# Performance work log

Hardware: AMD Instinct MI355X
Metric: run time of the kernel (lower is better)

The kernel has to match this reference:

```python
import jax, jax.numpy as jnp
import numpy as np

B, SEQ, DIM = 2, 2048, 1024
HEADS, DIM_HEAD = 16, 64
INNER = HEADS * DIM_HEAD
SCALE = DIM_HEAD ** -0.5


def rotate_half(x):
    # pair consecutive dims (d r) with r=2: (x1, x2) -> (-x2, x1)
    xp = x.reshape(*x.shape[:-1], -1, 2)
    x1, x2 = xp[..., 0], xp[..., 1]
    return jnp.stack((-x2, x1), axis=-1).reshape(x.shape)


def apply_rotary_emb(freqs, t):
    # freqs: [n, rot_dim] angles; t: [b, h, n, d]
    rot_dim = freqs.shape[-1]
    t_rot, t_pass = t[..., :rot_dim], t[..., rot_dim:]
    t_rot = t_rot * jnp.cos(freqs) + rotate_half(t_rot) * jnp.sin(freqs)
    return jnp.concatenate([t_rot, t_pass], axis=-1)


def setup_inputs() -> dict:
    key = jax.random.key(0)
    ks = jax.random.split(key, 4)
    x = jax.random.normal(ks[0], (B, SEQ, DIM), dtype=jnp.float32)
    mask = jnp.ones((B, SEQ), dtype=bool)
    rotary_pos_emb = jax.random.uniform(ks[1], (SEQ, DIM_HEAD), dtype=jnp.float32)
    Wqkv = jax.random.normal(ks[2], (DIM, 3 * INNER), dtype=jnp.float32) * 0.02
    Wout = jax.random.normal(ks[3], (INNER, DIM), dtype=jnp.float32) * 0.02
    bout = jnp.zeros((DIM,), dtype=jnp.float32)
    return {"x": x, "mask": mask, "rotary_pos_emb": rotary_pos_emb,
            "Wqkv": Wqkv, "Wout": Wout, "bout": bout}


def reference(x, mask, rotary_pos_emb, Wqkv, Wout, bout):
    b, n, _ = x.shape
    qkv = x @ Wqkv                                   # [b, n, 3*inner]
    q, k, v = jnp.split(qkv, 3, axis=-1)

    def to_heads(t):
        return t.reshape(b, n, HEADS, DIM_HEAD).transpose(0, 2, 1, 3)  # [b,h,n,d]

    q, k, v = to_heads(q), to_heads(k), to_heads(v)
    freqs = rotary_pos_emb[:n, :]
    # NB: original applies rotary to q, k AND v
    q = apply_rotary_emb(freqs, q)
    k = apply_rotary_emb(freqs, k)
    v = apply_rotary_emb(freqs, v)
    q = q * SCALE

    dots = jnp.einsum('bhid,bhjd->bhij', q, k)       # [b,h,n,n]
    mask_value = -jnp.finfo(dots.dtype).max
    pad = mask[:, None, None, :]                     # [b,1,1,n] keep where True
    dots = jnp.where(pad, dots, mask_value)
    idx = jnp.arange(n)
    causal = idx[None, :] > idx[:, None]             # j >= i + (j-i+1) with i==j==n
    dots = jnp.where(causal[None, None], mask_value, dots)

    attn = jax.nn.softmax(dots, axis=-1)
    out = jnp.einsum('bhij,bhjd->bhid', attn, v)     # [b,h,n,d]
    out = out.transpose(0, 2, 1, 3).reshape(b, n, INNER)
    return out @ Wout + bout
```

## Files before the change

### kernel.cpp

```cpp
#include <hip/hip_runtime.h>
#include <hip/hip_bf16.h>
#include <stdint.h>

#define DEVI __device__ __forceinline__

typedef __bf16 bf16x8 __attribute__((ext_vector_type(8)));
typedef float f32x4 __attribute__((ext_vector_type(4)));
typedef float f32x16 __attribute__((ext_vector_type(16)));

static constexpr int SEQ = 2048;
static constexpr int DIM = 1024;
static constexpr int HEADS = 16;
static constexpr int NQKV = 3072;
static constexpr int MROWS = 4096;
static constexpr float QSCALE = 0.125f;
static constexpr float LOG2E = 1.4426950408889634f;

DEVI unsigned short f2bf(float f) {
  unsigned int u = __builtin_bit_cast(unsigned int, f);
  u += 0x7FFFu + ((u >> 16) & 1u);
  return (unsigned short)(u >> 16);
}

DEVI bf16x8 ld8(const unsigned short* p) {
  return __builtin_bit_cast(bf16x8, *(const uint4*)p);
}

DEVI f32x4 mfma16(bf16x8 a, bf16x8 b, f32x4 c) {
  return __builtin_amdgcn_mfma_f32_16x16x32_bf16(a, b, c, 0, 0, 0);
}

DEVI f32x16 mfma32(bf16x8 a, bf16x8 b, f32x16 c) {
  return __builtin_amdgcn_mfma_f32_32x32x16_bf16(a, b, c, 0, 0, 0);
}

DEVI void load_lds16(const void* g, void* l) {
  __builtin_amdgcn_global_load_lds((const __attribute__((address_space(1))) void*)g,
                                   (__attribute__((address_space(3))) void*)l,
                                   16, 0, 0);
}

DEVI int swz(int row, int kelem) {
  return row * 64 + (kelem ^ ((row & 7) << 3));
}

DEVI unsigned cvtpk(float lo, float hi) {
  unsigned r;
  asm("v_cvt_pk_bf16_f32 %0, %1, %2" : "=v"(r) : "v"(lo), "v"(hi));
  return r;
}

DEVI void pl32swap(unsigned& a, unsigned& b) {
  asm volatile("v_permlane32_swap_b32 %0, %1" : "+v"(a), "+v"(b));
}
DEVI float xhalf_max(float v) { return fmaxf(v, __shfl_xor(v, 32)); }
DEVI float xhalf_sum(float v) { return v + __shfl_xor(v, 32); }

DEVI void transpose_tile(const float* __restrict__ in, unsigned short* __restrict__ out,
                         int Kd, int Nd, int bx, int by, int tid,
                         unsigned short (*T)[68]) {
  const int n0 = bx * 64, k0 = by * 64;
  const int rr = tid >> 4, cc = (tid & 15) * 4;
#pragma unroll
  for (int p = 0; p < 4; ++p) {
    const int r = p * 16 + rr;
    float4 f = *(const float4*)(in + (size_t)(k0 + r) * Nd + n0 + cc);
    T[r][cc + 0] = f2bf(f.x);
    T[r][cc + 1] = f2bf(f.y);
    T[r][cc + 2] = f2bf(f.z);
    T[r][cc + 3] = f2bf(f.w);
  }
  __syncthreads();
#pragma unroll
  for (int p = 0; p < 4; ++p) {
    const int rn = p * 16 + rr;
    ushort4 v;
    v.x = T[cc + 0][rn];
    v.y = T[cc + 1][rn];
    v.z = T[cc + 2][rn];
    v.w = T[cc + 3][rn];
    *(ushort4*)(out + (size_t)(n0 + rn) * Kd + k0 + cc) = v;
  }
}

__global__ __launch_bounds__(256) void k_prep(
    const float* __restrict__ x, unsigned short* __restrict__ xb,
    const float* __restrict__ rope, float* __restrict__ cosb, float* __restrict__ sinb,
    const float* __restrict__ Wqkv, unsigned short* __restrict__ wqkvt,
    const float* __restrict__ Wout, unsigned short* __restrict__ woutt) {
  __shared__ unsigned short T[64][68];
  const int bid = blockIdx.x, tid = threadIdx.x;
  if (bid < 4096) {
    const int i = bid * 256 + tid;
    float4 f = *(const float4*)(x + (size_t)i * 4);
    ushort4 v;
    v.x = f2bf(f.x); v.y = f2bf(f.y); v.z = f2bf(f.z); v.w = f2bf(f.w);
    *(ushort4*)(xb + (size_t)i * 4) = v;
  } else if (bid < 4608) {
    const int i = (bid - 4096) * 256 + tid;
    float f = rope[i];
    cosb[i] = cosf(f);
    sinb[i] = sinf(f);
  } else if (bid < 5376) {
    const int idx = bid - 4608;
    transpose_tile(Wqkv, wqkvt, DIM, NQKV, idx % 48, idx / 48, tid, T);
  } else {
    const int idx = bid - 5376;
    transpose_tile(Wout, woutt, DIM, DIM, idx % 16, idx / 16, tid, T);
  }
}

DEVI void gemm_mainloop64(const unsigned short* __restrict__ A,
                          const unsigned short* __restrict__ B, int K,
                          int m0, int n0,
                          unsigned short* As, unsigned short* Bs,
                          f32x4 (&acc)[4][4]) {
  const int lane = threadIdx.x & 63;
  const int wid = threadIdx.x >> 6;
  const int wm = wid >> 1, wn = wid & 1;
  const int rsub = lane >> 3;
  const int ksw = ((lane & 7) ^ rsub) * 8;
  for (int kt = 0; kt < K; kt += 64) {
    __syncthreads();
#pragma unroll
    for (int i = 0; i < 4; ++i) {
      const int chunk = wid * 4 + i;
      const int row = chunk * 8 + rsub;
      load_lds16(A + (size_t)(m0 + row) * K + kt + ksw, As + chunk * 512);
      load_lds16(B + (size_t)(n0 + row) * K + kt + ksw, Bs + chunk * 512);
    }
    __syncthreads();
#pragma unroll
    for (int kk = 0; kk < 2; ++kk) {
      bf16x8 af[4], bfv[4];
#pragma unroll
      for (int mi = 0; mi < 4; ++mi)
        af[mi] = ld8(&As[swz(wm * 64 + mi * 16 + (lane & 15),
                             kk * 32 + 8 * (lane >> 4))]);
#pragma unroll
      for (int ni = 0; ni < 4; ++ni)
        bfv[ni] = ld8(&Bs[swz(wn * 64 + ni * 16 + (lane & 15),
                              kk * 32 + 8 * (lane >> 4))]);
#pragma unroll
      for (int mi = 0; mi < 4; ++mi)
#pragma unroll
        for (int ni = 0; ni < 4; ++ni)
          acc[mi][ni] = mfma16(af[mi], bfv[ni], acc[mi][ni]);
    }
  }
}

__global__ __launch_bounds__(512, 1) void k_gemm_qkv(
    const unsigned short* __restrict__ xb, const unsigned short* __restrict__ wt,
    const float* __restrict__ cosb, const float* __restrict__ sinb,
    unsigned short* __restrict__ qb, unsigned short* __restrict__ kb,
    unsigned short* __restrict__ vb) {
  __shared__ __align__(16) unsigned short Ab[2][2][8192];
  __shared__ __align__(16) unsigned short Bb[2][12288];
  const int tid = threadIdx.x, lane = tid & 63, wid = tid >> 6;
  const int wm = wid >> 2, wn = wid & 3;
  const int m0 = blockIdx.x * 256, n0 = blockIdx.y * 192;
  const int la15 = lane & 15, l16 = lane >> 4;
  const int pS0 = tid, pS1 = tid + 512;
  const int sr0 = pS0 >> 3, sr1 = pS1 >> 3;
  const int sc0 = ((pS0 & 7) ^ (sr0 & 7)) * 8, sc1 = ((pS1 & 7) ^ (sr1 & 7)) * 8;
  const int bsr = tid >> 3;
  const int bsc = ((tid & 7) ^ (bsr & 7)) * 8;

  auto stageA = [&](int h, int s) {
    const unsigned short* src = xb + (size_t)(m0 + h * 128) * DIM + s * 64;
    unsigned short* dst = &Ab[s & 1][h][0];
    load_lds16(src + (size_t)sr0 * DIM + sc0, dst + pS0 * 8);
    load_lds16(src + (size_t)sr1 * DIM + sc1, dst + pS1 * 8);
  };
  auto stageB3 = [&](int t, int s) {
    const unsigned short* src = wt + (size_t)(n0 + t * 64 + bsr) * DIM + s * 64;
    load_lds16(src + bsc, &Bb[s & 1][t * 4096] + tid * 8);
  };

  f32x4 acc[8][3] = {};
  stageA(0, 0); stageA(1, 0); stageB3(0, 0); stageB3(1, 0); stageB3(2, 0);
  stageA(0, 1); stageA(1, 1); stageB3(0, 1); stageB3(1, 1); stageB3(2, 1);

#pragma unroll 1
  for (int s = 0; s < 16; ++s) {
    const unsigned short* Ah = &Ab[s & 1][wm][0];
    const unsigned short* Bh = &Bb[s & 1][0];
    const int rb = wn * 48;
    bf16x8 bfr[3][2];
#pragma unroll
    for (int q = 0; q < 4; ++q) {
      if (q == 0) {
        if (s == 0)       asm volatile("s_waitcnt vmcnt(7)" ::: "memory");
        else if (s == 15) asm volatile("s_waitcnt vmcnt(0)" ::: "memory");
        else              asm volatile("s_waitcnt vmcnt(3)" ::: "memory");
        __syncthreads();
      }
      if (q == 2) __syncthreads();
      bf16x8 afr[2][2];
      if (q == 0) {
#pragma unroll
        for (int ni = 0; ni < 3; ++ni)
#pragma unroll
          for (int kk = 0; kk < 2; ++kk)
            bfr[ni][kk] = ld8(&Bh[swz(rb + ni * 16 + la15, kk * 32 + 8 * l16)]);
      }
#pragma unroll
      for (int mi = 0; mi < 2; ++mi)
#pragma unroll
        for (int kk = 0; kk < 2; ++kk)
          afr[mi][kk] = ld8(&Ah[swz(q * 32 + mi * 16 + la15, kk * 32 + 8 * l16)]);
      if (q == 0)      { if (s >= 1 && s + 1 < 16) stageA(0, s + 1); }
      else if (q == 1) { if (s >= 1 && s + 1 < 16) stageA(1, s + 1); }
      else if (q == 2) { if (s + 2 < 16) stageB3(0, s + 2); }
      else             { if (s + 2 < 16) { stageB3(1, s + 2); stageB3(2, s + 2); } }
      asm volatile("s_waitcnt lgkmcnt(0)" ::: "memory");
      __builtin_amdgcn_sched_barrier(0);
      __builtin_amdgcn_s_setprio(1);
#pragma unroll
      for (int kk = 0; kk < 2; ++kk)
#pragma unroll
        for (int mi = 0; mi < 2; ++mi)
#pragma unroll
          for (int ni = 0; ni < 3; ++ni)
            acc[2 * q + mi][ni] = mfma16(afr[mi][kk], bfr[ni][kk], acc[2 * q + mi][ni]);
      __builtin_amdgcn_s_setprio(0);
    }
  }

#pragma unroll
  for (int mq = 0; mq < 8; ++mq) {
#pragma unroll
    for (int ni = 0; ni < 3; ++ni) {
      const int ng = n0 + wn * 48 + ni * 16 + la15;
      const int d = ng & 63;
      const int part = ng >> 10;
      const int h = (ng & 1023) >> 6;
      const int mg0 = m0 + wm * 128 + mq * 16 + 4 * l16;
      const int s0 = mg0 & (SEQ - 1), b = mg0 >> 11;
      const size_t bh = (size_t)(b * HEADS + h);
      if (part == 2) {
        ushort4 vv;
#pragma unroll
        for (int r = 0; r < 4; ++r) {
          const int s = s0 + r;
          float v = acc[mq][ni][r];
          float p = __shfl_xor(v, 1);
          float cv = cosb[(s << 6) + d], sv = sinb[(s << 6) + d];
          float rot = v * cv + ((d & 1) ? p : -p) * sv;
          ((unsigned short*)&vv)[r] = f2bf(rot);
        }
        *(ushort4*)(vb + (bh * 64 + d) * SEQ + s0) = vv;
      } else {
#pragma unroll
        for (int r = 0; r < 4; ++r) {
          const int s = s0 + r;
          float v = acc[mq][ni][r];
          float p = __shfl_xor(v, 1);
          float cv = cosb[(s << 6) + d], sv = sinb[(s << 6) + d];
          float rot = v * cv + ((d & 1) ? p : -p) * sv;
          if (part == 0) {
            qb[(bh * SEQ + s) * 64 + d] = f2bf(rot * (QSCALE * LOG2E));
          } else {
            kb[(bh * SEQ + s) * 64 + d] = f2bf(rot);
          }
        }
      }
    }
  }
}

__global__ __launch_bounds__(256) void k_flash(
    const unsigned short* __restrict__ qb, const unsigned short* __restrict__ kb,
    const unsigned short* __restrict__ vtb, unsigned short* __restrict__ ao) {
  __shared__ __align__(16) unsigned short Ks[2][2][4096];
  __shared__ __align__(16) unsigned short Vt[2][4096];
  const int bh = blockIdx.x;
  const int qt = 31 - blockIdx.y;
  const int tid = threadIdx.x, lane = tid & 63, wid = tid >> 6;
  const int wq = wid >> 1, wk = wid & 1;
  const int la31 = lane & 31, h = lane >> 5;
  const unsigned short* kbh = kb + (size_t)bh * SEQ * 64;
  const unsigned short* vbh = vtb + (size_t)bh * 64 * SEQ;
  const int b = bh >> 4, hh = bh & 15;
  const int sslot = ((lane & 7) ^ (lane >> 3)) * 8;
  float* mrg = (float*)&Ks[0][0][0];
  const int mbase = wq * 2176;

  auto stageK = [&](int buf, int t) {
    const int kv0 = t * 64;
#pragma unroll
    for (int i = 0; i < 4; ++i) {
      const int chunk = wq * 4 + i;
      const int row = chunk * 8 + (lane >> 3);
      load_lds16(kbh + ((size_t)(kv0 + row) << 6) + sslot, &Ks[buf][wk][chunk * 512]);
    }
  };
  auto stageV = [&](int t) {
    const int kv0 = t * 64;
#pragma unroll
    for (int i = 0; i < 4; ++i) {
      const int chunk = wq * 4 + i;
      const int row = chunk * 8 + (lane >> 3);
      load_lds16(vbh + (size_t)row * SEQ + kv0 + sslot, &Vt[wk][chunk * 512]);
    }
  };

  const int q0 = qt * 64 + wq * 32;
  const int qr = q0 + la31;
  const unsigned short* qp = qb + ((size_t)bh * SEQ + qr) * 64;
  bf16x8 qf0 = ld8(qp + 0 + 8 * h);
  bf16x8 qf1 = ld8(qp + 16 + 8 * h);
  bf16x8 qf2 = ld8(qp + 32 + 8 * h);
  bf16x8 qf3 = ld8(qp + 48 + 8 * h);

  f32x16 o0 = {}, o1 = {};
  float m = -1e30f, l = 0.f;
  const int nkv = qt + 1;
  const int nst = (nkv + 1) >> 1;

  if (wk < nkv) stageK(0, wk);
#pragma unroll 1
  for (int st = 0; st < nst; ++st) {
    const int cur = st & 1;
    const int t = 2 * st + wk;
    const bool live = (t < nkv);
    __syncthreads();
    if (live) stageV(t);
    { const int tn = 2 * (st + 1) + wk; if (tn < nkv) stageK(cur ^ 1, tn); }

    f32x16 st0 = {}, st1 = {};
    bf16x8 pa0, pa1, pa2, pa3;
    if (live) {
      const int kv0 = t * 64;
      const unsigned short* Kc = &Ks[cur][wk][0];
      __builtin_amdgcn_s_setprio(1);
#pragma unroll
      for (int ks = 0; ks < 4; ++ks) {
        bf16x8 qk = (ks == 0) ? qf0 : (ks == 1) ? qf1 : (ks == 2) ? qf2 : qf3;
        st0 = mfma32(ld8(&Kc[swz(la31, 16 * ks + 8 * h)]), qk, st0);
        st1 = mfma32(ld8(&Kc[swz(32 + la31, 16 * ks + 8 * h)]), qk, st1);
      }
      __builtin_amdgcn_s_setprio(0);
      if (kv0 + 63 > q0) {
#pragma unroll
        for (int r = 0; r < 16; ++r) {
          const int kvo = (r & 3) + 8 * (r >> 2) + 4 * h;
          st0[r] = (kv0 + kvo > qr) ? -1e30f : st0[r];
          st1[r] = (kv0 + 32 + kvo > qr) ? -1e30f : st1[r];
        }
      }
      float a8[8];
#pragma unroll
      for (int i = 0; i < 8; ++i)
        a8[i] = fmaxf(fmaxf(st0[i], st0[i + 8]), fmaxf(st1[i], st1[i + 8]));
      float a4_0 = fmaxf(a8[0], a8[4]), a4_1 = fmaxf(a8[1], a8[5]);
      float a4_2 = fmaxf(a8[2], a8[6]), a4_3 = fmaxf(a8[3], a8[7]);
      float pmax = fmaxf(fmaxf(a4_0, a4_1), fmaxf(a4_2, a4_3));
      const bool nor = __all(pmax <= m + 8.f);
      float scl = 1.f;
      if (!nor) {
        const float rowmax = xhalf_max(pmax);
        const float mnew = fmaxf(m, rowmax);
        scl = exp2f(m - mnew);
        m = mnew;
      }
#pragma unroll
      for (int r = 0; r < 16; ++r) {
        st0[r] = exp2f(st0[r] - m);
        st1[r] = exp2f(st1[r] - m);
      }
      float s8[8];
#pragma unroll
      for (int i = 0; i < 8; ++i)
        s8[i] = (st0[i] + st0[i + 8]) + (st1[i] + st1[i + 8]);
      float s4_0 = s8[0] + s8[4], s4_1 = s8[1] + s8[5];
      float s4_2 = s8[2] + s8[6], s4_3 = s8[3] + s8[7];
      float psum = (s4_0 + s4_1) + (s4_2 + s4_3);
      const float rowsum = xhalf_sum(psum);
      if (nor) {
        l += rowsum;
      } else {
        l = l * scl + rowsum;
#pragma unroll
        for (int r = 0; r < 16; ++r) { o0[r] *= scl; o1[r] *= scl; }
      }
      unsigned w0 = cvtpk(st0[0], st0[1]),   w1 = cvtpk(st0[2], st0[3]);
      unsigned w2 = cvtpk(st0[4], st0[5]),   w3 = cvtpk(st0[6], st0[7]);
      unsigned w4 = cvtpk(st0[8], st0[9]),   w5 = cvtpk(st0[10], st0[11]);
      unsigned w6 = cvtpk(st0[12], st0[13]), w7 = cvtpk(st0[14], st0[15]);
      pl32swap(w0, w2); pl32swap(w1, w3); pl32swap(w4, w6); pl32swap(w5, w7);
      pa0 = __builtin_bit_cast(bf16x8, (uint4){w0, w1, w2, w3});
      pa1 = __builtin_bit_cast(bf16x8, (uint4){w4, w5, w6, w7});
      unsigned x0 = cvtpk(st1[0], st1[1]),   x1 = cvtpk(st1[2], st1[3]);
      unsigned x2 = cvtpk(st1[4], st1[5]),   x3 = cvtpk(st1[6], st1[7]);
      unsigned x4 = cvtpk(st1[8], st1[9]),   x5 = cvtpk(st1[10], st1[11]);
      unsigned x6 = cvtpk(st1[12], st1[13]), x7 = cvtpk(st1[14], st1[15]);
      pl32swap(x0, x2); pl32swap(x1, x3); pl32swap(x4, x6); pl32swap(x5, x7);
      pa2 = __builtin_bit_cast(bf16x8, (uint4){x0, x1, x2, x3});
      pa3 = __builtin_bit_cast(bf16x8, (uint4){x4, x5, x6, x7});
    }
    __syncthreads();
    if (live) {
      const unsigned short* Vc = &Vt[wk][0];
      __builtin_amdgcn_s_setprio(1);
      o0 = mfma32(ld8(&Vc[swz(la31, 0 + 8 * h)]), pa0, o0);
      o0 = mfma32(ld8(&Vc[swz(la31, 16 + 8 * h)]), pa1, o0);
      o0 = mfma32(ld8(&Vc[swz(la31, 32 + 8 * h)]), pa2, o0);
      o0 = mfma32(ld8(&Vc[swz(la31, 48 + 8 * h)]), pa3, o0);
      o1 = mfma32(ld8(&Vc[swz(32 + la31, 0 + 8 * h)]), pa0, o1);
      o1 = mfma32(ld8(&Vc[swz(32 + la31, 16 + 8 * h)]), pa1, o1);
      o1 = mfma32(ld8(&Vc[swz(32 + la31, 32 + 8 * h)]), pa2, o1);
      o1 = mfma32(ld8(&Vc[swz(32 + la31, 48 + 8 * h)]), pa3, o1);
      __builtin_amdgcn_s_setprio(0);
    }
  }

  __syncthreads();
  if (wk == 1) {
#pragma unroll
    for (int s = 0; s < 8; ++s) {
      f32x4 c;
      if (s < 4) { c[0]=o0[4*s]; c[1]=o0[4*s+1]; c[2]=o0[4*s+2]; c[3]=o0[4*s+3]; }
      else       { c[0]=o1[4*(s-4)]; c[1]=o1[4*(s-4)+1]; c[2]=o1[4*(s-4)+2]; c[3]=o1[4*(s-4)+3]; }
      *(f32x4*)&mrg[mbase + lane * 32 + 4 * (s ^ (lane & 7))] = c;
    }
    mrg[mbase + 2048 + lane] = m;
    mrg[mbase + 2112 + lane] = l;
  }
  __syncthreads();
  if (wk == 0) {
    const float m1 = mrg[mbase + 2048 + lane];
    const float l1 = mrg[mbase + 2112 + lane];
    const float mM = fmaxf(m, m1);
    const float sc0 = exp2f(m - mM), sc1 = exp2f(m1 - mM);
    const float lt = l * sc0 + l1 * sc1;
    const float rl = __builtin_amdgcn_rcpf(lt);
    unsigned short* aor = ao + ((size_t)(b * SEQ + qr)) * 1024 + hh * 64;
#pragma unroll
    for (int s = 0; s < 8; ++s) {
      f32x4 c = *(const f32x4*)&mrg[mbase + lane * 32 + 4 * (s ^ (lane & 7))];
      float v0, v1, v2, v3;
      if (s < 4) {
        v0 = (o0[4*s]   * sc0 + c[0] * sc1) * rl;
        v1 = (o0[4*s+1] * sc0 + c[1] * sc1) * rl;
        v2 = (o0[4*s+2] * sc0 + c[2] * sc1) * rl;
        v3 = (o0[4*s+3] * sc0 + c[3] * sc1) * rl;
      } else {
        v0 = (o1[4*(s-4)]   * sc0 + c[0] * sc1) * rl;
        v1 = (o1[4*(s-4)+1] * sc0 + c[1] * sc1) * rl;
        v2 = (o1[4*(s-4)+2] * sc0 + c[2] * sc1) * rl;
        v3 = (o1[4*(s-4)+3] * sc0 + c[3] * sc1) * rl;
      }
      uint2 uv;
      uv.x = cvtpk(v0, v1);
      uv.y = cvtpk(v2, v3);
      *(uint2*)(aor + (s < 4 ? 8 * s : 32 + 8 * (s - 4)) + 4 * h) = uv;
    }
  }
}

__global__ __launch_bounds__(256) void k_gemm_out(
    const unsigned short* __restrict__ ao, const unsigned short* __restrict__ wt,
    const float* __restrict__ bout, float* __restrict__ out) {
  __shared__ __align__(16) unsigned short As[128 * 64];
  __shared__ __align__(16) unsigned short Bs[128 * 64];
  const int m0 = blockIdx.x * 128, n0 = blockIdx.y * 128;
  f32x4 acc[4][4] = {};
  gemm_mainloop64(ao, wt, DIM, m0, n0, As, Bs, acc);
  const int lane = threadIdx.x & 63, wid = threadIdx.x >> 6;
  const int wm = wid >> 1, wn = wid & 1;
#pragma unroll
  for (int mi = 0; mi < 4; ++mi) {
#pragma unroll
    for (int ni = 0; ni < 4; ++ni) {
      const int ng = n0 + wn * 64 + ni * 16 + (lane & 15);
      const float bn = bout[ng];
#pragma unroll
      for (int r = 0; r < 4; ++r) {
        const int mg = m0 + wm * 64 + mi * 16 + 4 * (lane >> 4) + r;
        out[(size_t)mg * DIM + ng] = acc[mi][ni][r] + bn;
      }
    }
  }
}

extern "C" void kernel_launch(void* const* d_in, const int* in_sizes, int n_in,
                              void* d_out, int out_size, void* d_ws, size_t ws_size,
                              hipStream_t stream) {
  const float* x    = (const float*)d_in[0];
  const float* rope = (const float*)d_in[2];
  const float* Wqkv = (const float*)d_in[3];
  const float* Wout = (const float*)d_in[4];
  const float* bout = (const float*)d_in[5];
  float* out = (float*)d_out;

  char* ws = (char*)d_ws;
  unsigned short* xb    = (unsigned short*)(ws + 0);
  unsigned short* wqkvt = (unsigned short*)(ws + 8388608);
  unsigned short* woutt = (unsigned short*)(ws + 14680064);
  float*          cosb  = (float*)(ws + 16777216);
  float*          sinb  = (float*)(ws + 17301504);
  unsigned short* qbuf  = (unsigned short*)(ws + 17825792);
  unsigned short* kbuf  = (unsigned short*)(ws + 26214400);
  unsigned short* vbuf  = (unsigned short*)(ws + 34603008);
  unsigned short* aob   = (unsigned short*)(ws + 42991616);

  k_prep<<<5632, 256, 0, stream>>>(x, xb, rope, cosb, sinb, Wqkv, wqkvt, Wout, woutt);
  k_gemm_qkv<<<dim3(16, 16), 512, 0, stream>>>(xb, wqkvt, cosb, sinb,
                                               qbuf, kbuf, vbuf);
  k_flash<<<dim3(32, 32), 256, 0, stream>>>(qbuf, kbuf, vbuf, aob);
  k_gemm_out<<<dim3(MROWS / 128, DIM / 128), 256, 0, stream>>>(aob, woutt, bout, out);
}
```

Measured before the change: 120.9 us.

## Split long causal flash tiles across two blocks and merge partials in a new kernel

The upper 16 query tiles (which have the most KV tiles under the causal mask) are now each split into two blocks that process halves of the KV range. Each half writes a bf16 partial output plus row max and sum into reused workspace buffers. A new merge kernel combines the two partials into the attention output. The goal is to balance work across blocks and cut the long-tail critical path. The cost is an extra launch, extra global traffic, and bf16 rounding of the unnormalized partials.

```diff
diff --git a/kernel.cpp b/kernel.cpp
--- a/kernel.cpp
+++ b/kernel.cpp
@@ -272,11 +272,20 @@
 
 __global__ __launch_bounds__(256) void k_flash(
     const unsigned short* __restrict__ qb, const unsigned short* __restrict__ kb,
-    const unsigned short* __restrict__ vtb, unsigned short* __restrict__ ao) {
+    const unsigned short* __restrict__ vtb, unsigned short* __restrict__ ao,
+    unsigned short* __restrict__ pO, float* __restrict__ pM,
+    float* __restrict__ pL) {
   __shared__ __align__(16) unsigned short Ks[2][2][4096];
   __shared__ __align__(16) unsigned short Vt[2][4096];
   const int bh = blockIdx.x;
-  const int qt = 31 - blockIdx.y;
+  const int y = blockIdx.y;
+  const bool split = (y < 32);
+  const int qt = split ? (31 - (y >> 1)) : (47 - y);
+  const int half = y & 1;
+  const int nkv = qt + 1;
+  const int nlo = (nkv + 1) >> 1;
+  const int t0 = (split && half) ? nlo : 0;
+  const int nkvl = split ? (half ? nkv - nlo : nlo) : nkv;
   const int tid = threadIdx.x, lane = tid & 63, wid = tid >> 6;
   const int wq = wid >> 1, wk = wid & 1;
   const int la31 = lane & 31, h = lane >> 5;
@@ -316,24 +325,24 @@
 
   f32x16 o0 = {}, o1 = {};
   float m = -1e30f, l = 0.f;
-  const int nkv = qt + 1;
-  const int nst = (nkv + 1) >> 1;
-
-  if (wk < nkv) stageK(0, wk);
+  const int nstl = (nkvl + 1) >> 1;
+
+  if (wk < nkvl) stageK(0, t0 + wk);
 #pragma unroll 1
-  for (int st = 0; st < nst; ++st) {
-    const int cur = st & 1;
-    const int t = 2 * st + wk;
-    const bool live = (t < nkv);
+  for (int stp = 0; stp < nstl; ++stp) {
+    const int cur = stp & 1;
+    const int tl = 2 * stp + wk;
+    const bool live = (tl < nkvl);
+    const int tg = t0 + tl;
     __syncthreads();
-    if (live) stageV(t);
-    { const int tn = 2 * (st + 1) + wk; if (tn < nkv) stageK(cur ^ 1, tn); }
-
-    f32x16 st0 = {}, st1 = {};
+    if (live) stageV(tg);
+    { const int tn = 2 * (stp + 1) + wk; if (tn < nkvl) stageK(cur ^ 1, t0 + tn); }
+
     bf16x8 pa0, pa1, pa2, pa3;
     if (live) {
-      const int kv0 = t * 64;
+      const int kv0 = tg * 64;
       const unsigned short* Kc = &Ks[cur][wk][0];
+      f32x16 st0 = {}, st1 = {};
       __builtin_amdgcn_s_setprio(1);
 #pragma unroll
       for (int ks = 0; ks < 4; ++ks) {
@@ -435,29 +444,94 @@
     const float mM = fmaxf(m, m1);
     const float sc0 = exp2f(m - mM), sc1 = exp2f(m1 - mM);
     const float lt = l * sc0 + l1 * sc1;
-    const float rl = __builtin_amdgcn_rcpf(lt);
-    unsigned short* aor = ao + ((size_t)(b * SEQ + qr)) * 1024 + hh * 64;
-#pragma unroll
-    for (int s = 0; s < 8; ++s) {
-      f32x4 c = *(const f32x4*)&mrg[mbase + lane * 32 + 4 * (s ^ (lane & 7))];
-      float v0, v1, v2, v3;
-      if (s < 4) {
-        v0 = (o0[4*s]   * sc0 + c[0] * sc1) * rl;
-        v1 = (o0[4*s+1] * sc0 + c[1] * sc1) * rl;
-        v2 = (o0[4*s+2] * sc0 + c[2] * sc1) * rl;
-        v3 = (o0[4*s+3] * sc0 + c[3] * sc1) * rl;
-      } else {
-        v0 = (o1[4*(s-4)]   * sc0 + c[0] * sc1) * rl;
-        v1 = (o1[4*(s-4)+1] * sc0 + c[1] * sc1) * rl;
-        v2 = (o1[4*(s-4)+2] * sc0 + c[2] * sc1) * rl;
-        v3 = (o1[4*(s-4)+3] * sc0 + c[3] * sc1) * rl;
-      }
-      uint2 uv;
-      uv.x = cvtpk(v0, v1);
-      uv.y = cvtpk(v2, v3);
-      *(uint2*)(aor + (s < 4 ? 8 * s : 32 + 8 * (s - 4)) + 4 * h) = uv;
-    }
-  }
+    if (!split) {
+      const float rl = __builtin_amdgcn_rcpf(lt);
+      unsigned short* aor = ao + ((size_t)(b * SEQ + qr)) * 1024 + hh * 64;
+#pragma unroll
+      for (int s = 0; s < 8; ++s) {
+        f32x4 c = *(const f32x4*)&mrg[mbase + lane * 32 + 4 * (s ^ (lane & 7))];
+        float v0, v1, v2, v3;
+        if (s < 4) {
+          v0 = (o0[4*s]   * sc0 + c[0] * sc1) * rl;
+          v1 = (o0[4*s+1] * sc0 + c[1] * sc1) * rl;
+          v2 = (o0[4*s+2] * sc0 + c[2] * sc1) * rl;
+          v3 = (o0[4*s+3] * sc0 + c[3] * sc1) * rl;
+        } else {
+          v0 = (o1[4*(s-4)]   * sc0 + c[0] * sc1) * rl;
+          v1 = (o1[4*(s-4)+1] * sc0 + c[1] * sc1) * rl;
+          v2 = (o1[4*(s-4)+2] * sc0 + c[2] * sc1) * rl;
+          v3 = (o1[4*(s-4)+3] * sc0 + c[3] * sc1) * rl;
+        }
+        uint2 uv;
+        uv.x = cvtpk(v0, v1);
+        uv.y = cvtpk(v2, v3);
+        *(uint2*)(aor + (s < 4 ? 8 * s : 32 + 8 * (s - 4)) + 4 * h) = uv;
+      }
+    } else {
+      const int tI = bh * 16 + (qt - 16);
+      const int rloc = wq * 32 + la31;
+      unsigned short* por = pO + (size_t)(tI * 2 + half) * 4096 + rloc * 64;
+      pM[(tI * 2 + half) * 64 + rloc] = mM;
+      pL[(tI * 2 + half) * 64 + rloc] = lt;
+#pragma unroll
+      for (int s = 0; s < 8; ++s) {
+        f32x4 c = *(const f32x4*)&mrg[mbase + lane * 32 + 4 * (s ^ (lane & 7))];
+        float v0, v1, v2, v3;
+        if (s < 4) {
+          v0 = o0[4*s]   * sc0 + c[0] * sc1;
+          v1 = o0[4*s+1] * sc0 + c[1] * sc1;
+          v2 = o0[4*s+2] * sc0 + c[2] * sc1;
+          v3 = o0[4*s+3] * sc0 + c[3] * sc1;
+        } else {
+          v0 = o1[4*(s-4)]   * sc0 + c[0] * sc1;
+          v1 = o1[4*(s-4)+1] * sc0 + c[1] * sc1;
+          v2 = o1[4*(s-4)+2] * sc0 + c[2] * sc1;
+          v3 = o1[4*(s-4)+3] * sc0 + c[3] * sc1;
+        }
+        uint2 uv;
+        uv.x = cvtpk(v0, v1);
+        uv.y = cvtpk(v2, v3);
+        *(uint2*)(por + (s < 4 ? 8 * s : 32 + 8 * (s - 4)) + 4 * h) = uv;
+      }
+    }
+  }
+}
+
+__global__ __launch_bounds__(256) void k_fmerge(
+    const unsigned short* __restrict__ pO, const float* __restrict__ pM,
+    const float* __restrict__ pL, unsigned short* __restrict__ ao) {
+  const int tI = blockIdx.x;
+  const int bh = tI >> 4, qt = 16 + (tI & 15);
+  const int b = bh >> 4, hh = bh & 15;
+  const int t = threadIdx.x;
+  const int r = t >> 2, c0 = (t & 3) * 16;
+  const float m0 = pM[(2 * tI) * 64 + r], m1 = pM[(2 * tI + 1) * 64 + r];
+  const float l0 = pL[(2 * tI) * 64 + r], l1 = pL[(2 * tI + 1) * 64 + r];
+  const float mM = fmaxf(m0, m1);
+  const float sc0 = exp2f(m0 - mM), sc1 = exp2f(m1 - mM);
+  const float rl = __builtin_amdgcn_rcpf(l0 * sc0 + l1 * sc1);
+  const unsigned short* p0 = pO + (size_t)(2 * tI) * 4096 + r * 64 + c0;
+  const unsigned short* p1 = pO + (size_t)(2 * tI + 1) * 4096 + r * 64 + c0;
+  uint4 ua[2] = { *(const uint4*)p0, *(const uint4*)(p0 + 8) };
+  uint4 ub[2] = { *(const uint4*)p1, *(const uint4*)(p1 + 8) };
+  uint4 uo[2];
+#pragma unroll
+  for (int w = 0; w < 2; ++w) {
+#pragma unroll
+    for (int k2 = 0; k2 < 4; ++k2) {
+      const unsigned da = ((const unsigned*)&ua[w])[k2];
+      const unsigned db = ((const unsigned*)&ub[w])[k2];
+      const float alo = __builtin_bit_cast(float, da << 16);
+      const float ahi = __builtin_bit_cast(float, da & 0xFFFF0000u);
+      const float blo = __builtin_bit_cast(float, db << 16);
+      const float bhi = __builtin_bit_cast(float, db & 0xFFFF0000u);
+      ((unsigned*)&uo[w])[k2] = cvtpk((alo * sc0 + blo * sc1) * rl,
+                                      (ahi * sc0 + bhi * sc1) * rl);
+    }
+  }
+  unsigned short* dst = ao + ((size_t)(b * SEQ + qt * 64 + r)) * 1024 + hh * 64 + c0;
+  *(uint4*)dst = uo[0];
+  *(uint4*)(dst + 8) = uo[1];
 }
 
 __global__ __launch_bounds__(256) void k_gemm_out(
@@ -505,10 +579,14 @@
   unsigned short* kbuf  = (unsigned short*)(ws + 26214400);
   unsigned short* vbuf  = (unsigned short*)(ws + 34603008);
   unsigned short* aob   = (unsigned short*)(ws + 42991616);
+  unsigned short* pO    = xb;
+  float*          pM    = cosb;
+  float*          pL    = sinb;
 
   k_prep<<<5632, 256, 0, stream>>>(x, xb, rope, cosb, sinb, Wqkv, wqkvt, Wout, woutt);
   k_gemm_qkv<<<dim3(16, 16), 512, 0, stream>>>(xb, wqkvt, cosb, sinb,
                                                qbuf, kbuf, vbuf);
-  k_flash<<<dim3(32, 32), 256, 0, stream>>>(qbuf, kbuf, vbuf, aob);
+  k_flash<<<dim3(32, 48), 256, 0, stream>>>(qbuf, kbuf, vbuf, aob, pO, pM, pL);
+  k_fmerge<<<512, 256, 0, stream>>>(pO, pM, pL, aob);
   k_gemm_out<<<dim3(MROWS / 128, DIM / 128), 256, 0, stream>>>(aob, woutt, bout, out);
 }
```

Result: slower. 127.0 us (+5.0%).
